# Kernel tuning notes

Measured on AMD Instinct MI355X. Metric: run time of the kernel, lower is better.

The kernel has to match this reference:

```python
import jax, jax.numpy as jnp
import numpy as np

B, N, E = 8, 50000, 800000
IN_DIM, OUT_DIM = 64, 64


def setup_inputs() -> dict:
    key = jax.random.key(0)
    k_x, k_src, k_dst, k_ws, k_bs, k_wn, k_bn = jax.random.split(key, 7)
    x = jax.random.normal(k_x, (B, N, IN_DIM), dtype=jnp.float32)
    src = jax.random.randint(k_src, (E,), 0, N, dtype=jnp.int64)
    dst = jax.random.randint(k_dst, (E,), 0, N, dtype=jnp.int64)
    edge_index = jnp.stack([src, dst], axis=1)  # (E, 2)
    # nn.Linear init: U(-1/sqrt(in_dim), 1/sqrt(in_dim))
    bound = 1.0 / np.sqrt(IN_DIM)
    W_self = jax.random.uniform(k_ws, (OUT_DIM, IN_DIM), jnp.float32, -bound, bound)
    b_self = jax.random.uniform(k_bs, (OUT_DIM,), jnp.float32, -bound, bound)
    W_neigh = jax.random.uniform(k_wn, (OUT_DIM, IN_DIM), jnp.float32, -bound, bound)
    b_neigh = jax.random.uniform(k_bn, (OUT_DIM,), jnp.float32, -bound, bound)
    return {"x": x, "edge_index": edge_index, "W_self": W_self, "b_self": b_self,
            "W_neigh": W_neigh, "b_neigh": b_neigh}


def reference(x, edge_index, W_self, b_self, W_neigh, b_neigh):
    # x: (B, N, D); edge_index: (E, 2) [src, dst], shared topology across batch
    src = edge_index[:, 0]
    dst = edge_index[:, 1]
    # scatter-add neighbor aggregation, vectorized over batch
    agg = jnp.zeros_like(x).at[:, dst].add(x[:, src])  # (B, N, D)
    h_self = jnp.einsum('bnd,od->bno', x, W_self) + b_self
    h_neigh = jnp.einsum('bnd,od->bno', agg, W_neigh) + b_neigh
    return jax.nn.relu(h_self + h_neigh)
```

## Files before the change

### kernel.cpp

```cpp
#include <hip/hip_runtime.h>

#define Bn 8
#define Nn 50000
#define En 800000
#define Dd 64
#define AS 136
#define CAP 64

typedef __attribute__((ext_vector_type(8))) unsigned short ushort8;
typedef __attribute__((ext_vector_type(8))) __bf16 bf16x8;
typedef __attribute__((ext_vector_type(4))) float floatx4;

__device__ __forceinline__ unsigned short f2bf(float f) {
  unsigned int u = __builtin_bit_cast(unsigned int, f);
  u = (u + 0x7FFFu + ((u >> 16) & 1u)) >> 16;
  return (unsigned short)u;
}

__global__ __launch_bounds__(256) void k_fconv(const float* __restrict__ x,
                                               unsigned short* __restrict__ xb,
                                               const int* __restrict__ ei,
                                               int* __restrict__ deg,
                                               unsigned short* __restrict__ bucket) {
  const size_t gid = (size_t)blockIdx.x * 256 + threadIdx.x;
  const size_t i = gid * 4;
  const float4 v = *(const float4*)(x + i);
  ushort4 o;
  o.x = f2bf(v.x); o.y = f2bf(v.y); o.z = f2bf(v.z); o.w = f2bf(v.w);
  *(ushort4*)(xb + i) = o;
  if (gid < En) {
    const int d = ei[2 * gid + 1];
    const int s = ei[2 * gid + 0];
    const int p = atomicAdd(&deg[d], 1);
    if (p < CAP) bucket[(d << 6) + p] = (unsigned short)s;
  }
}

__global__ __launch_bounds__(256, 4) void k_main(
    const unsigned short* __restrict__ xb, const unsigned short* __restrict__ bucket,
    const int* __restrict__ deg, const float* __restrict__ Ws,
    const float* __restrict__ bs, const float* __restrict__ Wn,
    const float* __restrict__ bn, float* __restrict__ out) {
  __shared__ __align__(16) unsigned short Wt[64 * AS];
  __shared__ __align__(16) unsigned short A[64 * AS];
  __shared__ float bias[64];
  __shared__ int eidx[4][64];

  const int tid = threadIdx.x;
  const int b = blockIdx.x & 7;
  const int node0 = (blockIdx.x >> 3) * 64;
  const int wave = tid >> 6;
  const int lane = tid & 63;

  for (int idx = tid; idx < 64 * 128; idx += 256) {
    int o = idx >> 7, k = idx & 127;
    float v = (k < 64) ? Ws[o * 64 + k] : Wn[o * 64 + (k - 64)];
    Wt[o * AS + k] = f2bf(v);
  }
  if (tid < 64) bias[tid] = bs[tid] + bn[tid];

  const int slot = lane >> 3;
  const int li = lane & 7;
  const int ebase = lane & 56;
  const size_t xb_base = (size_t)b * Nn * Dd;

  for (int g = 0; g < 2; ++g) {
    const int nl = wave * 16 + g * 8 + slot;
    const int node = node0 + nl;
    float acc[8] = {0.f, 0.f, 0.f, 0.f, 0.f, 0.f, 0.f, 0.f};
    if (node < Nn) {
      const int cnt = min(deg[node], CAP);
      const unsigned short* bkt = bucket + (node << 6);
      int base = 0;
      for (; base + 8 <= cnt; base += 8) {
        eidx[wave][ebase + li] = bkt[base + li];
        #pragma unroll
        for (int t = 0; t < 8; ++t) {
          const int s = eidx[wave][ebase + t];
          const uint4 v = *(const uint4*)(xb + xb_base + (size_t)s * Dd + li * 8);
          const unsigned int* w = (const unsigned int*)&v;
          #pragma unroll
          for (int j = 0; j < 4; ++j) {
            acc[2 * j] += __builtin_bit_cast(float, w[j] << 16);
            acc[2 * j + 1] += __builtin_bit_cast(float, w[j] & 0xFFFF0000u);
          }
        }
      }
      const int rem = cnt - base;
      if (rem > 0) {
        if (li < rem) eidx[wave][ebase + li] = bkt[base + li];
        for (int t = 0; t < rem; ++t) {
          const int s = eidx[wave][ebase + t];
          const uint4 v = *(const uint4*)(xb + xb_base + (size_t)s * Dd + li * 8);
          const unsigned int* w = (const unsigned int*)&v;
          #pragma unroll
          for (int j = 0; j < 4; ++j) {
            acc[2 * j] += __builtin_bit_cast(float, w[j] << 16);
            acc[2 * j + 1] += __builtin_bit_cast(float, w[j] & 0xFFFF0000u);
          }
        }
      }
      const uint4 sv = *(const uint4*)(xb + xb_base + (size_t)node * Dd + li * 8);
      *(uint4*)&A[nl * AS + li * 8] = sv;
    } else {
      const uint4 z = make_uint4(0, 0, 0, 0);
      *(uint4*)&A[nl * AS + li * 8] = z;
    }
    ushort8 av;
    #pragma unroll
    for (int j = 0; j < 8; ++j) av[j] = f2bf(acc[j]);
    *(ushort8*)&A[nl * AS + 64 + li * 8] = av;
  }
  __syncthreads();

  const int col = lane & 15;
  const int quad = lane >> 4;
  bf16x8 af[4];
  {
    const unsigned short* arow = &A[(wave * 16 + col) * AS + quad * 8];
    #pragma unroll
    for (int k = 0; k < 4; ++k)
      af[k] = __builtin_bit_cast(bf16x8, *(const ushort8*)(arow + k * 32));
  }
  #pragma unroll
  for (int t = 0; t < 4; ++t) {
    floatx4 acc = {0.f, 0.f, 0.f, 0.f};
    const unsigned short* brow = &Wt[(t * 16 + col) * AS + quad * 8];
    #pragma unroll
    for (int k = 0; k < 4; ++k) {
      bf16x8 bf = __builtin_bit_cast(bf16x8, *(const ushort8*)(brow + k * 32));
      acc = __builtin_amdgcn_mfma_f32_16x16x32_bf16(af[k], bf, acc, 0, 0, 0);
    }
    const float bv = bias[t * 16 + col];
    #pragma unroll
    for (int r = 0; r < 4; ++r) {
      const int node = node0 + wave * 16 + quad * 4 + r;
      if (node < Nn) {
        float v = acc[r] + bv;
        out[((size_t)b * Nn + node) * Dd + t * 16 + col] = v > 0.f ? v : 0.f;
      }
    }
  }
}

#define OFF_XB 0ull
#define OFF_DEG 51200000ull
#define OFF_BKT 51400000ull
#define WS_NEED 57800000ull

extern "C" void kernel_launch(void* const* d_in, const int* in_sizes, int n_in,
                              void* d_out, int out_size, void* d_ws,
                              size_t ws_size, hipStream_t stream) {
  const float* x = (const float*)d_in[0];
  const int* ei = (const int*)d_in[1];
  const float* Ws = (const float*)d_in[2];
  const float* bs = (const float*)d_in[3];
  const float* Wn = (const float*)d_in[4];
  const float* bn = (const float*)d_in[5];
  float* out = (float*)d_out;

  if (ws_size < WS_NEED) return;

  char* ws = (char*)d_ws;
  unsigned short* xb = (unsigned short*)(ws + OFF_XB);
  int* deg = (int*)(ws + OFF_DEG);
  unsigned short* bucket = (unsigned short*)(ws + OFF_BKT);

  hipMemsetAsync(deg, 0, Nn * sizeof(int), stream);
  k_fconv<<<(Bn * Nn * Dd / 4) / 256, 256, 0, stream>>>(x, xb, ei, deg, bucket);
  const int ntiles = (Nn + 63) / 64;
  k_main<<<ntiles * Bn, 256, 0, stream>>>(xb, bucket, deg, Ws, bs, Wn, bn, out);
}
```

Baseline: 337.9 us.

## Swizzle LDS tiles, pad buckets with sentinel, vectorize bucket index loads

```diff
diff --git a/kernel.cpp b/kernel.cpp
--- a/kernel.cpp
+++ b/kernel.cpp
@@ -4,7 +4,6 @@
 #define Nn 50000
 #define En 800000
 #define Dd 64
-#define AS 136
 #define CAP 64
 
 typedef __attribute__((ext_vector_type(8))) unsigned short ushort8;
@@ -15,6 +14,10 @@
   unsigned int u = __builtin_bit_cast(unsigned int, f);
   u = (u + 0x7FFFu + ((u >> 16) & 1u)) >> 16;
   return (unsigned short)u;
+}
+
+__device__ __forceinline__ int swz(int row, int byte_in_row) {
+  return (row * 256 + byte_in_row) ^ ((row & 7) << 4);
 }
 
 __global__ __launch_bounds__(256) void k_fconv(const float* __restrict__ x,
@@ -29,87 +32,76 @@
   o.x = f2bf(v.x); o.y = f2bf(v.y); o.z = f2bf(v.z); o.w = f2bf(v.w);
   *(ushort4*)(xb + i) = o;
   if (gid < En) {
-    const int d = ei[2 * gid + 1];
-    const int s = ei[2 * gid + 0];
-    const int p = atomicAdd(&deg[d], 1);
-    if (p < CAP) bucket[(d << 6) + p] = (unsigned short)s;
+    const int2 e = *(const int2*)(ei + 2 * gid);
+    const int p = atomicAdd(&deg[e.y], 1);
+    if (p < CAP) bucket[(e.y << 6) + p] = (unsigned short)e.x;
   }
 }
 
-__global__ __launch_bounds__(256, 4) void k_main(
+__global__ __launch_bounds__(256, 5) void k_main(
     const unsigned short* __restrict__ xb, const unsigned short* __restrict__ bucket,
     const int* __restrict__ deg, const float* __restrict__ Ws,
     const float* __restrict__ bs, const float* __restrict__ Wn,
     const float* __restrict__ bn, float* __restrict__ out) {
-  __shared__ __align__(16) unsigned short Wt[64 * AS];
-  __shared__ __align__(16) unsigned short A[64 * AS];
-  __shared__ float bias[64];
-  __shared__ int eidx[4][64];
+  __shared__ __align__(16) unsigned short Wt[64 * 128];
+  __shared__ __align__(16) unsigned short A[64 * 128];
 
   const int tid = threadIdx.x;
   const int b = blockIdx.x & 7;
   const int node0 = (blockIdx.x >> 3) * 64;
   const int wave = tid >> 6;
   const int lane = tid & 63;
+  char* Ac = (char*)A;
+  char* Wc = (char*)Wt;
 
-  for (int idx = tid; idx < 64 * 128; idx += 256) {
-    int o = idx >> 7, k = idx & 127;
-    float v = (k < 64) ? Ws[o * 64 + k] : Wn[o * 64 + (k - 64)];
-    Wt[o * AS + k] = f2bf(v);
+  for (int i = tid; i < 64 * 32; i += 256) {
+    const int o = i >> 5;
+    const int k = (i & 31) * 4;
+    const float4 wv = (k < 64) ? *(const float4*)(Ws + o * 64 + k)
+                               : *(const float4*)(Wn + o * 64 + (k - 64));
+    ushort4 u;
+    u.x = f2bf(wv.x); u.y = f2bf(wv.y); u.z = f2bf(wv.z); u.w = f2bf(wv.w);
+    *(ushort4*)(Wc + swz(o, k * 2)) = u;
   }
-  if (tid < 64) bias[tid] = bs[tid] + bn[tid];
 
   const int slot = lane >> 3;
   const int li = lane & 7;
-  const int ebase = lane & 56;
-  const size_t xb_base = (size_t)b * Nn * Dd;
+  const size_t xb_base = (size_t)b * Nn * Dd + (size_t)(li * 8);
 
   for (int g = 0; g < 2; ++g) {
     const int nl = wave * 16 + g * 8 + slot;
     const int node = node0 + nl;
     float acc[8] = {0.f, 0.f, 0.f, 0.f, 0.f, 0.f, 0.f, 0.f};
     if (node < Nn) {
+      const uint4 sv = *(const uint4*)(xb + xb_base + (size_t)node * Dd);
       const int cnt = min(deg[node], CAP);
       const unsigned short* bkt = bucket + (node << 6);
-      int base = 0;
-      for (; base + 8 <= cnt; base += 8) {
-        eidx[wave][ebase + li] = bkt[base + li];
+      const int nch = (cnt + 7) >> 3;
+      for (int c = 0; c < nch; ++c) {
+        const uint4 e = *(const uint4*)(bkt + c * 8);
+        const unsigned int ew[4] = {e.x, e.y, e.z, e.w};
         #pragma unroll
         for (int t = 0; t < 8; ++t) {
-          const int s = eidx[wave][ebase + t];
-          const uint4 v = *(const uint4*)(xb + xb_base + (size_t)s * Dd + li * 8);
-          const unsigned int* w = (const unsigned int*)&v;
+          unsigned int s = (ew[t >> 1] >> ((t & 1) * 16)) & 0xFFFFu;
+          const float m = (s < (unsigned)Nn) ? 1.0f : 0.0f;
+          s = min(s, (unsigned)(Nn - 1));
+          const uint4 v = *(const uint4*)(xb + xb_base + (size_t)s * Dd);
+          const unsigned int w[4] = {v.x, v.y, v.z, v.w};
           #pragma unroll
           for (int j = 0; j < 4; ++j) {
-            acc[2 * j] += __builtin_bit_cast(float, w[j] << 16);
-            acc[2 * j + 1] += __builtin_bit_cast(float, w[j] & 0xFFFF0000u);
+            acc[2 * j]     = fmaf(m, __builtin_bit_cast(float, w[j] << 16), acc[2 * j]);
+            acc[2 * j + 1] = fmaf(m, __builtin_bit_cast(float, w[j] & 0xFFFF0000u), acc[2 * j + 1]);
           }
         }
       }
-      const int rem = cnt - base;
-      if (rem > 0) {
-        if (li < rem) eidx[wave][ebase + li] = bkt[base + li];
-        for (int t = 0; t < rem; ++t) {
-          const int s = eidx[wave][ebase + t];
-          const uint4 v = *(const uint4*)(xb + xb_base + (size_t)s * Dd + li * 8);
-          const unsigned int* w = (const unsigned int*)&v;
-          #pragma unroll
-          for (int j = 0; j < 4; ++j) {
-            acc[2 * j] += __builtin_bit_cast(float, w[j] << 16);
-            acc[2 * j + 1] += __builtin_bit_cast(float, w[j] & 0xFFFF0000u);
-          }
-        }
-      }
-      const uint4 sv = *(const uint4*)(xb + xb_base + (size_t)node * Dd + li * 8);
-      *(uint4*)&A[nl * AS + li * 8] = sv;
+      *(uint4*)(Ac + swz(nl, li * 16)) = sv;
     } else {
-      const uint4 z = make_uint4(0, 0, 0, 0);
-      *(uint4*)&A[nl * AS + li * 8] = z;
+      *(uint4*)(Ac + swz(nl, li * 16)) = make_uint4(0, 0, 0, 0);
     }
     ushort8 av;
     #pragma unroll
     for (int j = 0; j < 8; ++j) av[j] = f2bf(acc[j]);
-    *(ushort8*)&A[nl * AS + 64 + li * 8] = av;
+    *(ushort8*)(Ac + swz(nl, 128 + li * 16)) = av;
   }
   __syncthreads();
 
@@ -117,27 +109,28 @@
   const int quad = lane >> 4;
   bf16x8 af[4];
   {
-    const unsigned short* arow = &A[(wave * 16 + col) * AS + quad * 8];
+    const int row = wave * 16 + col;
     #pragma unroll
     for (int k = 0; k < 4; ++k)
-      af[k] = __builtin_bit_cast(bf16x8, *(const ushort8*)(arow + k * 32));
+      af[k] = __builtin_bit_cast(bf16x8, *(const ushort8*)(Ac + swz(row, quad * 16 + k * 64)));
   }
   #pragma unroll
   for (int t = 0; t < 4; ++t) {
     floatx4 acc = {0.f, 0.f, 0.f, 0.f};
-    const unsigned short* brow = &Wt[(t * 16 + col) * AS + quad * 8];
+    const int row = t * 16 + col;
     #pragma unroll
     for (int k = 0; k < 4; ++k) {
-      bf16x8 bf = __builtin_bit_cast(bf16x8, *(const ushort8*)(brow + k * 32));
+      bf16x8 bf = __builtin_bit_cast(bf16x8, *(const ushort8*)(Wc + swz(row, quad * 16 + k * 64)));
       acc = __builtin_amdgcn_mfma_f32_16x16x32_bf16(af[k], bf, acc, 0, 0, 0);
     }
-    const float bv = bias[t * 16 + col];
+    const int o = t * 16 + col;
+    const float bv = bs[o] + bn[o];
     #pragma unroll
     for (int r = 0; r < 4; ++r) {
       const int node = node0 + wave * 16 + quad * 4 + r;
       if (node < Nn) {
         float v = acc[r] + bv;
-        out[((size_t)b * Nn + node) * Dd + t * 16 + col] = v > 0.f ? v : 0.f;
+        out[((size_t)b * Nn + node) * Dd + o] = v > 0.f ? v : 0.f;
       }
     }
   }
@@ -167,6 +160,7 @@
   unsigned short* bucket = (unsigned short*)(ws + OFF_BKT);
 
   hipMemsetAsync(deg, 0, Nn * sizeof(int), stream);
+  hipMemsetAsync(bucket, 0xFF, (size_t)Nn * CAP * sizeof(unsigned short), stream);
   k_fconv<<<(Bn * Nn * Dd / 4) / 256, 256, 0, stream>>>(x, xb, ei, deg, bucket);
   const int ntiles = (Nn + 63) / 64;
   k_main<<<ntiles * Bn, 256, 0, stream>>>(xb, bucket, deg, Ws, bs, Wn, bn, out);
```

After: 328.9 us. -2.7%, faster.
